# Performance work log

Hardware: AMD Instinct MI355X
Metric: run time of the kernel (lower is better)

The kernel has to match this reference:

```python
import jax, jax.numpy as jnp
import numpy as np

DIM = 1024
LN_EPS = 1e-5

def _layernorm(x, w, b):
    m = jnp.mean(x, axis=-1, keepdims=True)
    v = jnp.mean((x - m) ** 2, axis=-1, keepdims=True)
    return (x - m) * jax.lax.rsqrt(v + LN_EPS) * w + b

def _linear(x, w, b):
    # torch Linear: w is (out, in)
    return jnp.einsum('bsd,od->bso', x, w) + b

def setup_inputs() -> dict:
    key = jax.random.key(0)
    ks = jax.random.split(key, 8)
    d = DIM
    s = 0.02
    return {
        'x': jax.random.normal(ks[0], (4, 4096, d), dtype=jnp.float32),
        'ln1_w': jnp.ones((d,), jnp.float32), 'ln1_b': jnp.zeros((d,), jnp.float32),
        'ln2_w': jnp.ones((d,), jnp.float32), 'ln2_b': jnp.zeros((d,), jnp.float32),
        'gate_w': jax.random.normal(ks[1], (d, d), jnp.float32) * s,
        'gate_b': jnp.zeros((d,), jnp.float32),
        'val_w': jax.random.normal(ks[2], (d, d), jnp.float32) * s,
        'val_b': jnp.zeros((d,), jnp.float32),
        'ffn1_w': jax.random.normal(ks[3], (4 * d, d), jnp.float32) * s,
        'ffn1_b': jnp.zeros((4 * d,), jnp.float32),
        'ffn2_w': jax.random.normal(ks[4], (d, 4 * d), jnp.float32) * s,
        'ffn2_b': jnp.zeros((d,), jnp.float32),
    }

def reference(x, ln1_w, ln1_b, ln2_w, ln2_b, gate_w, gate_b, val_w, val_b, ffn1_w, ffn1_b, ffn2_w, ffn2_b):
    batch, seq_len, dim = x.shape
    h = _layernorm(x, ln1_w, ln1_b)
    g = jax.nn.sigmoid(_linear(h, gate_w, gate_b))
    v = _linear(h, val_w, val_b)
    cumsum_v = jnp.cumsum(g * v, axis=1)
    cumsum_g = jnp.cumsum(g, axis=1) + 1e-6
    position = jnp.arange(1, seq_len + 1, dtype=x.dtype)[None, :, None]  # [1,S,1]
    mem = cumsum_v / (jnp.sqrt(cumsum_g) * jnp.sqrt(position / seq_len + 0.1))
    x = x + mem
    h2 = _layernorm(x, ln2_w, ln2_b)
    ff = _linear(jax.nn.gelu(_linear(h2, ffn1_w, ffn1_b), approximate=False), ffn2_w, ffn2_b)
    return x + ff
```

## Files before the change

### kernel.cpp

```cpp
#include <hip/hip_runtime.h>
#include <cstdint>
#include <cstddef>

#define DIMD 1024
#define SEQ  4096
#define BATCH 4
#define MTOT (BATCH*SEQ)
#define NCHUNK 64
#define CLEN   64

typedef __attribute__((ext_vector_type(8))) short short8;
typedef __attribute__((ext_vector_type(4))) float floatx4;

__device__ __forceinline__ unsigned short f2bf(float f){
  unsigned u = __float_as_uint(f);
  u += 0x7fffu + ((u >> 16) & 1u);
  return (unsigned short)(u >> 16);
}
__device__ __forceinline__ float bf2f(unsigned short u){
  return __uint_as_float((unsigned)u << 16);
}

__device__ __forceinline__ void async16(const void* g, void* l){
  __builtin_amdgcn_global_load_lds(
      (const __attribute__((address_space(1))) void*)g,
      (__attribute__((address_space(3))) void*)l, 16, 0, 0);
}

__global__ void f32_to_bf16_kernel(const float* __restrict__ in,
                                   unsigned short* __restrict__ out, int n){
  int i = (blockIdx.x * 256 + threadIdx.x) * 4;
  if (i < n){
    float4 v = *(const float4*)(in + i);
    uint2 o;
    o.x = (unsigned)f2bf(v.x) | ((unsigned)f2bf(v.y) << 16);
    o.y = (unsigned)f2bf(v.z) | ((unsigned)f2bf(v.w) << 16);
    *(uint2*)(out + i) = o;
  }
}

__global__ __launch_bounds__(256)
void ln_kernel(const float* __restrict__ X, const float* __restrict__ w,
               const float* __restrict__ b, unsigned short* __restrict__ H){
  const int row = blockIdx.x;
  const int tid = threadIdx.x;
  const float4 xv = ((const float4*)(X + (size_t)row * DIMD))[tid];
  float s  = xv.x + xv.y + xv.z + xv.w;
  float ss = xv.x*xv.x + xv.y*xv.y + xv.z*xv.z + xv.w*xv.w;
  #pragma unroll
  for (int o = 32; o; o >>= 1){
    s  += __shfl_down(s, o);
    ss += __shfl_down(ss, o);
  }
  __shared__ float ps[4], pss[4], mv[2];
  const int wid = tid >> 6, lane = tid & 63;
  if (lane == 0){ ps[wid] = s; pss[wid] = ss; }
  __syncthreads();
  if (tid == 0){
    float S1 = ps[0]+ps[1]+ps[2]+ps[3];
    float S2 = pss[0]+pss[1]+pss[2]+pss[3];
    float m = S1 * (1.0f / DIMD);
    float var = S2 * (1.0f / DIMD) - m*m;
    mv[0] = m; mv[1] = rsqrtf(var + 1e-5f);
  }
  __syncthreads();
  const float m = mv[0], rs = mv[1];
  const float4 wv = ((const float4*)w)[tid];
  const float4 bv = ((const float4*)b)[tid];
  float o0 = (xv.x - m) * rs * wv.x + bv.x;
  float o1 = (xv.y - m) * rs * wv.y + bv.y;
  float o2 = (xv.z - m) * rs * wv.z + bv.z;
  float o3 = (xv.w - m) * rs * wv.w + bv.w;
  uint2 o;
  o.x = (unsigned)f2bf(o0) | ((unsigned)f2bf(o1) << 16);
  o.y = (unsigned)f2bf(o2) | ((unsigned)f2bf(o3) << 16);
  ((uint2*)(H + (size_t)row * DIMD))[tid] = o;
}

template<int EPI>
__global__ __launch_bounds__(512, 2)
void gemm256(const unsigned short* __restrict__ A, int lda,
             const unsigned short* __restrict__ Bw, int ldb,
             const float* __restrict__ bias, const float* __restrict__ bias2,
             void* __restrict__ OutP, void* __restrict__ Out2P,
             int ldc, int grid_n, int K)
{
  __shared__ char lds[2][2][32*1024];
  const int tid = threadIdx.x;
  const int bid = ((int)blockIdx.x & 7) * ((int)gridDim.x >> 3) + ((int)blockIdx.x >> 3);
  const int bm = bid / grid_n, bn = bid % grid_n;
  const int row0 = bm * 256, col0 = bn * 256;
  const int wid = tid >> 6, lane = tid & 63;
  const int wr = wid >> 2, wc = wid & 3;
  const int l15 = lane & 15, rq = lane >> 4, l7 = lane & 7;

  const int sbase = ((rq ^ (l7 & 3)) << 4) | (((l7 >> 2) & 1) << 6);

  const int st_r  = tid >> 3;
  const int st_sl = (tid & 7) ^ (st_r & 7);
  const int st_ldsoff = tid * 16;

  const unsigned short* Asrc = A  + (size_t)(row0 + st_r) * lda + st_sl * 8;
  const unsigned short* Bsrc = Bw + (size_t)(col0 + st_r) * ldb + st_sl * 8;

  floatx4 acc[8][4];
  #pragma unroll
  for (int m = 0; m < 8; ++m)
    #pragma unroll
    for (int n = 0; n < 4; ++n)
      acc[m][n] = (floatx4){0.f, 0.f, 0.f, 0.f};

  auto stage = [&](int buf, int k0){
    #pragma unroll
    for (int i = 0; i < 4; ++i)
      async16(Asrc + (size_t)(i * 64) * lda + k0, &lds[buf][0][i * 8192 + st_ldsoff]);
    #pragma unroll
    for (int i = 0; i < 4; ++i)
      async16(Bsrc + (size_t)(i * 64) * ldb + k0, &lds[buf][1][i * 8192 + st_ldsoff]);
  };

  const int nt = K >> 6;
  stage(0, 0);
  asm volatile("s_waitcnt vmcnt(0)" ::: "memory");
  asm volatile("s_barrier" ::: "memory");

  const int arow = wr * 128 + l15;
  const int brow = wc * 64 + l15;

  for (int t = 0; t < nt; ++t){
    const int buf = t & 1;
    const char* La = &lds[buf][0][0];
    const char* Lb = &lds[buf][1][0];
    short8 aF[4][2], bLo[2][2], bHi[2][2];

    #pragma unroll
    for (int mi = 0; mi < 4; ++mi)
      #pragma unroll
      for (int ks = 0; ks < 2; ++ks)
        aF[mi][ks] = *(const short8*)(La + (arow + mi*16) * 128 + (sbase ^ (ks << 6)));
    #pragma unroll
    for (int ni = 0; ni < 2; ++ni)
      #pragma unroll
      for (int ks = 0; ks < 2; ++ks)
        bLo[ni][ks] = *(const short8*)(Lb + (brow + ni*16) * 128 + (sbase ^ (ks << 6)));
    if (t + 1 < nt) stage(buf ^ 1, (t + 1) << 6);
    asm volatile("s_barrier" ::: "memory");
    __builtin_amdgcn_s_setprio(1);
    #pragma unroll
    for (int mi = 0; mi < 4; ++mi)
      #pragma unroll
      for (int ni = 0; ni < 2; ++ni)
        #pragma unroll
        for (int ks = 0; ks < 2; ++ks)
          acc[mi][ni] = __builtin_amdgcn_mfma_f32_16x16x32_bf16(
              aF[mi][ks], bLo[ni][ks], acc[mi][ni], 0, 0, 0);
    __builtin_amdgcn_s_setprio(0);
    asm volatile("s_barrier" ::: "memory");

    #pragma unroll
    for (int ni = 0; ni < 2; ++ni)
      #pragma unroll
      for (int ks = 0; ks < 2; ++ks)
        bHi[ni][ks] = *(const short8*)(Lb + (brow + (2+ni)*16) * 128 + (sbase ^ (ks << 6)));
    asm volatile("s_barrier" ::: "memory");
    __builtin_amdgcn_s_setprio(1);
    #pragma unroll
    for (int mi = 0; mi < 4; ++mi)
      #pragma unroll
      for (int ni = 0; ni < 2; ++ni)
        #pragma unroll
        for (int ks = 0; ks < 2; ++ks)
          acc[mi][2+ni] = __builtin_amdgcn_mfma_f32_16x16x32_bf16(
              aF[mi][ks], bHi[ni][ks], acc[mi][2+ni], 0, 0, 0);
    __builtin_amdgcn_s_setprio(0);
    asm volatile("s_barrier" ::: "memory");

    #pragma unroll
    for (int mi = 0; mi < 4; ++mi)
      #pragma unroll
      for (int ks = 0; ks < 2; ++ks)
        aF[mi][ks] = *(const short8*)(La + (arow + 64 + mi*16) * 128 + (sbase ^ (ks << 6)));
    asm volatile("s_barrier" ::: "memory");
    __builtin_amdgcn_s_setprio(1);
    #pragma unroll
    for (int mi = 0; mi < 4; ++mi)
      #pragma unroll
      for (int ni = 0; ni < 2; ++ni)
        #pragma unroll
        for (int ks = 0; ks < 2; ++ks)
          acc[4+mi][2+ni] = __builtin_amdgcn_mfma_f32_16x16x32_bf16(
              aF[mi][ks], bHi[ni][ks], acc[4+mi][2+ni], 0, 0, 0);
    #pragma unroll
    for (int mi = 0; mi < 4; ++mi)
      #pragma unroll
      for (int ni = 0; ni < 2; ++ni)
        #pragma unroll
        for (int ks = 0; ks < 2; ++ks)
          acc[4+mi][ni] = __builtin_amdgcn_mfma_f32_16x16x32_bf16(
              aF[mi][ks], bLo[ni][ks], acc[4+mi][ni], 0, 0, 0);
    __builtin_amdgcn_s_setprio(0);
    asm volatile("s_waitcnt vmcnt(0)" ::: "memory");
    asm volatile("s_barrier" ::: "memory");
  }

  if constexpr (EPI == 2 || EPI == 5){
    char* slab = &lds[0][0][0] + wid * 8192;
    unsigned short* dst; int colw; int ldout; bool sigm = false;
    const float* bsel;
    if constexpr (EPI == 5){
      const int c0 = col0 + wc * 64;
      if (c0 < 1024){ dst = (unsigned short*)OutP;  colw = c0;        bsel = bias;  sigm = true;  }
      else          { dst = (unsigned short*)Out2P; colw = c0 - 1024; bsel = bias2; sigm = false; }
      ldout = 1024;
    } else {
      dst = (unsigned short*)OutP; colw = col0 + wc * 64; bsel = bias; ldout = ldc;
    }
    const int rdrow = lane >> 3, rdsl = (lane & 7) * 16;
    #pragma unroll
    for (int m = 0; m < 8; ++m){
      #pragma unroll
      for (int n = 0; n < 4; ++n){
        const float bs = bsel[colw + n*16 + l15];
        #pragma unroll
        for (int j = 0; j < 4; ++j){
          const float val = acc[m][n][j] + bs;
          float r;
          if constexpr (EPI == 2){
            r = 0.5f * val * (1.f + erff(val * 0.70710678118f));
          } else {
            r = sigm ? (1.f / (1.f + expf(-val))) : val;
          }
          *(unsigned short*)(slab + (rq*4 + j) * 128 + (n*16 + l15) * 2) = f2bf(r);
        }
      }
      asm volatile("s_waitcnt lgkmcnt(0)" ::: "memory");
      uint4 w0 = *(const uint4*)(slab + rdrow * 128 + rdsl);
      uint4 w1 = *(const uint4*)(slab + (rdrow + 8) * 128 + rdsl);
      asm volatile("s_waitcnt lgkmcnt(0)" ::: "memory");
      const int growb = row0 + wr * 128 + m * 16;
      *(uint4*)((char*)(dst + (size_t)(growb + rdrow) * ldout + colw) + rdsl) = w0;
      *(uint4*)((char*)(dst + (size_t)(growb + rdrow + 8) * ldout + colw) + rdsl) = w1;
    }
  } else {
    #pragma unroll
    for (int n = 0; n < 4; ++n){
      const int col = col0 + wc * 64 + n * 16 + l15;
      const float bs = (EPI == 4) ? 0.f : bias[col];
      #pragma unroll
      for (int m = 0; m < 8; ++m){
        const int rowb = row0 + wr * 128 + m * 16 + rq * 4;
        #pragma unroll
        for (int j = 0; j < 4; ++j){
          const size_t o = (size_t)(rowb + j) * ldc + col;
          float* O = (float*)OutP;
          O[o] = acc[m][n][j] + bs + O[o];
        }
      }
    }
  }
}

__global__ __launch_bounds__(256)
void scan_sums(const unsigned short* __restrict__ G, const unsigned short* __restrict__ V,
               float* __restrict__ SG, float* __restrict__ SGV){
  const int bc = blockIdx.x;
  const int d  = blockIdx.y * 256 + threadIdx.x;
  const int b = bc >> 6, c = bc & 63;
  size_t base = ((size_t)b * SEQ + (size_t)c * CLEN) * DIMD + d;
  float sg = 0.f, sgv = 0.f;
  for (int i = 0; i < CLEN; ++i){
    float g = bf2f(G[base + (size_t)i * DIMD]);
    float v = bf2f(V[base + (size_t)i * DIMD]);
    sg += g; sgv += g * v;
  }
  SG[(size_t)bc * DIMD + d] = sg;
  SGV[(size_t)bc * DIMD + d] = sgv;
}

__global__ __launch_bounds__(256)
void scan_prefix(float* __restrict__ SG, float* __restrict__ SGV){
  const int b = blockIdx.x;
  const int d = blockIdx.y * 256 + threadIdx.x;
  float rg = 0.f, rgv = 0.f;
  for (int c = 0; c < NCHUNK; ++c){
    size_t i = ((size_t)(b * NCHUNK + c)) * DIMD + d;
    float tg = SG[i], tv = SGV[i];
    SG[i] = rg; SGV[i] = rgv;
    rg += tg; rgv += tv;
  }
}

__global__ __launch_bounds__(256)
void scan_final(const unsigned short* __restrict__ G, const unsigned short* __restrict__ V,
                const float* __restrict__ SG, const float* __restrict__ SGV,
                const float* __restrict__ X, float* __restrict__ X2){
  const int bc = blockIdx.x;
  const int d  = blockIdx.y * 256 + threadIdx.x;
  const int b = bc >> 6, c = bc & 63;
  size_t base = ((size_t)b * SEQ + (size_t)c * CLEN) * DIMD + d;
  float rg  = SG[(size_t)bc * DIMD + d];
  float rgv = SGV[(size_t)bc * DIMD + d];
  for (int i = 0; i < CLEN; ++i){
    size_t idx = base + (size_t)i * DIMD;
    float g = bf2f(G[idx]), v = bf2f(V[idx]);
    rg += g; rgv += g * v;
    int s = c * CLEN + i;
    float pf = (float)(s + 1) * (1.0f / SEQ) + 0.1f;
    float mem = rgv * rsqrtf((rg + 1e-6f) * pf);
    X2[idx] = X[idx] + mem;
  }
}

extern "C" void kernel_launch(void* const* d_in, const int* in_sizes, int n_in,
                              void* d_out, int out_size, void* d_ws, size_t ws_size,
                              hipStream_t stream)
{
  const float* x     = (const float*)d_in[0];
  const float* ln1w  = (const float*)d_in[1];
  const float* ln1b  = (const float*)d_in[2];
  const float* ln2w  = (const float*)d_in[3];
  const float* ln2b  = (const float*)d_in[4];
  const float* gatew = (const float*)d_in[5];
  const float* gateb = (const float*)d_in[6];
  const float* valw  = (const float*)d_in[7];
  const float* valb  = (const float*)d_in[8];
  const float* f1w   = (const float*)d_in[9];
  const float* f1b   = (const float*)d_in[10];
  const float* f2w   = (const float*)d_in[11];
  const float* f2b   = (const float*)d_in[12];
  float* out = (float*)d_out;

  const size_t MB = 1024u * 1024u;
  const size_t baseNeed = (size_t)(32+32+32+2+2+8+8)*MB + 2u*BATCH*NCHUNK*DIMD*4 + 4096;
  const bool bigT = (baseNeed + 64u*MB) <= ws_size;

  char* ws = (char*)d_ws;
  size_t off = 0;
  auto alloc = [&](size_t bytes) -> char* {
    char* p = ws + off; off += (bytes + 255) & ~(size_t)255; return p;
  };
  unsigned short* H  = (unsigned short*)alloc((size_t)MTOT * DIMD * 2);
  unsigned short* G  = (unsigned short*)alloc((size_t)MTOT * DIMD * 2);
  unsigned short* V  = (unsigned short*)alloc((size_t)MTOT * DIMD * 2);
  if (bigT) alloc(64u * MB);
  unsigned short* T  = G;
  unsigned short* WGV= (unsigned short*)alloc((size_t)2 * DIMD * DIMD * 2);
  unsigned short* W1 = (unsigned short*)alloc((size_t)4 * DIMD * DIMD * 2);
  unsigned short* W2 = (unsigned short*)alloc((size_t)4 * DIMD * DIMD * 2);
  float* SG  = (float*)alloc((size_t)BATCH * NCHUNK * DIMD * 4);
  float* SGV = (float*)alloc((size_t)BATCH * NCHUNK * DIMD * 4);

  if (off > ws_size) return;

  f32_to_bf16_kernel<<<DIMD*DIMD/1024, 256, 0, stream>>>(gatew, WGV, DIMD*DIMD);
  f32_to_bf16_kernel<<<DIMD*DIMD/1024, 256, 0, stream>>>(valw,  WGV + (size_t)DIMD*DIMD, DIMD*DIMD);
  f32_to_bf16_kernel<<<4*DIMD*DIMD/1024, 256, 0, stream>>>(f1w, W1, 4*DIMD*DIMD);
  f32_to_bf16_kernel<<<4*DIMD*DIMD/1024, 256, 0, stream>>>(f2w, W2, 4*DIMD*DIMD);

  ln_kernel<<<MTOT, 256, 0, stream>>>(x, ln1w, ln1b, H);

  gemm256<5><<<(MTOT/256)*(2048/256), 512, 0, stream>>>(
      H, DIMD, WGV, DIMD, gateb, valb, G, V, 2048, 2048/256, DIMD);

  scan_sums  <<<dim3(BATCH*NCHUNK, DIMD/256), 256, 0, stream>>>(G, V, SG, SGV);
  scan_prefix<<<dim3(BATCH, DIMD/256),        256, 0, stream>>>(SG, SGV);
  scan_final <<<dim3(BATCH*NCHUNK, DIMD/256), 256, 0, stream>>>(G, V, SG, SGV, x, out);

  ln_kernel<<<MTOT, 256, 0, stream>>>(out, ln2w, ln2b, H);

  if (bigT){
    gemm256<2><<<(MTOT/256)*(4096/256), 512, 0, stream>>>(
        H, DIMD, W1, DIMD, f1b, nullptr, T, nullptr, 4*DIMD, 4096/256, DIMD);
    gemm256<3><<<(MTOT/256)*(DIMD/256), 512, 0, stream>>>(
        T, 4*DIMD, W2, 4*DIMD, f2b, nullptr, out, nullptr, DIMD, DIMD/256, 4*DIMD);
  } else {
    for (int c = 0; c < 2; ++c){
      const unsigned short* W1c = W1 + (size_t)c * 2048 * DIMD;
      const unsigned short* W2c = W2 + (size_t)c * 2048;
      gemm256<2><<<(MTOT/256)*(2048/256), 512, 0, stream>>>(
          H, DIMD, W1c, DIMD, f1b + c*2048, nullptr, T, nullptr, 2048, 2048/256, DIMD);
      if (c == 0)
        gemm256<3><<<(MTOT/256)*(DIMD/256), 512, 0, stream>>>(
            T, 2048, W2c, 4*DIMD, f2b, nullptr, out, nullptr, DIMD, DIMD/256, 2048);
      else
        gemm256<4><<<(MTOT/256)*(DIMD/256), 512, 0, stream>>>(
            T, 2048, W2c, 4*DIMD, nullptr, nullptr, out, nullptr, DIMD, DIMD/256, 2048);
    }
  }
}
```

Measured before the change: 564.7 us.

## Use 4-stage LDS pipeline with K=32 tiles in bf16 GEMM

Restructures the GEMM main loop from a double-buffered K=64 tile with several barriers per iteration into a four-buffer ring of K=32 tiles, prefetching three tiles ahead and waiting with vmcnt(8) so global loads overlap more compute. Each iteration now uses one barrier and loads all A and B fragments before issuing the full 8x4 MFMA block. The LDS swizzle changes to fit the 64-byte rows, and the epilogue staging slab gains an XOR swizzle to cut bank conflicts. The risk is more loop iterations and barriers across the full K, and the redundant clamped tail prefetches at the end of the loop.

```diff
diff --git a/kernel.cpp b/kernel.cpp
--- a/kernel.cpp
+++ b/kernel.cpp
@@ -85,23 +85,19 @@
              void* __restrict__ OutP, void* __restrict__ Out2P,
              int ldc, int grid_n, int K)
 {
-  __shared__ char lds[2][2][32*1024];
+  __shared__ char lds[4 * 32768];
   const int tid = threadIdx.x;
   const int bid = ((int)blockIdx.x & 7) * ((int)gridDim.x >> 3) + ((int)blockIdx.x >> 3);
   const int bm = bid / grid_n, bn = bid % grid_n;
   const int row0 = bm * 256, col0 = bn * 256;
   const int wid = tid >> 6, lane = tid & 63;
   const int wr = wid >> 2, wc = wid & 3;
-  const int l15 = lane & 15, rq = lane >> 4, l7 = lane & 7;
-
-  const int sbase = ((rq ^ (l7 & 3)) << 4) | (((l7 >> 2) & 1) << 6);
-
-  const int st_r  = tid >> 3;
-  const int st_sl = (tid & 7) ^ (st_r & 7);
-  const int st_ldsoff = tid * 16;
-
-  const unsigned short* Asrc = A  + (size_t)(row0 + st_r) * lda + st_sl * 8;
-  const unsigned short* Bsrc = Bw + (size_t)(col0 + st_r) * ldb + st_sl * 8;
+  const int l15 = lane & 15, rq = lane >> 4;
+
+  const int st_sl = (tid & 3) ^ ((tid >> 3) & 3);
+  const unsigned short* Asrc = A  + (size_t)(row0 + (tid >> 2)) * lda + st_sl * 8;
+  const unsigned short* Bsrc = Bw + (size_t)(col0 + (tid >> 2)) * ldb + st_sl * 8;
+  const int st_off = tid * 16;
 
   floatx4 acc[8][4];
   #pragma unroll
@@ -110,101 +106,57 @@
     for (int n = 0; n < 4; ++n)
       acc[m][n] = (floatx4){0.f, 0.f, 0.f, 0.f};
 
-  auto stage = [&](int buf, int k0){
-    #pragma unroll
-    for (int i = 0; i < 4; ++i)
-      async16(Asrc + (size_t)(i * 64) * lda + k0, &lds[buf][0][i * 8192 + st_ldsoff]);
-    #pragma unroll
-    for (int i = 0; i < 4; ++i)
-      async16(Bsrc + (size_t)(i * 64) * ldb + k0, &lds[buf][1][i * 8192 + st_ldsoff]);
+  auto stage = [&](int buf, int kt){
+    const int k0 = kt << 5;
+    char* base = lds + buf * 32768;
+    #pragma unroll
+    for (int i = 0; i < 2; ++i)
+      async16(Asrc + (size_t)(i * 128) * lda + k0, base + i * 8192 + st_off);
+    #pragma unroll
+    for (int i = 0; i < 2; ++i)
+      async16(Bsrc + (size_t)(i * 128) * ldb + k0, base + 16384 + i * 8192 + st_off);
   };
 
-  const int nt = K >> 6;
-  stage(0, 0);
-  asm volatile("s_waitcnt vmcnt(0)" ::: "memory");
-  asm volatile("s_barrier" ::: "memory");
-
-  const int arow = wr * 128 + l15;
-  const int brow = wc * 64 + l15;
+  const int nt = K >> 5;
+  stage(0, 0); stage(1, 1); stage(2, 2);
 
   for (int t = 0; t < nt; ++t){
-    const int buf = t & 1;
-    const char* La = &lds[buf][0][0];
-    const char* Lb = &lds[buf][1][0];
-    short8 aF[4][2], bLo[2][2], bHi[2][2];
-
+    asm volatile("s_waitcnt vmcnt(8)" ::: "memory");
+    asm volatile("s_barrier" ::: "memory");
+    const char* La = lds + (t & 3) * 32768;
+    const char* Lb = La + 16384;
+
+    auto LD = [&](const char* Lp, int r)->short8 {
+      return *(const short8*)(Lp + (r << 6) + ((rq ^ ((r >> 1) & 3)) << 4));
+    };
+    short8 a0[4], a1[4], bv[4];
+    #pragma unroll
+    for (int mi = 0; mi < 4; ++mi) a0[mi] = LD(La, wr*128 + mi*16 + l15);
+    #pragma unroll
+    for (int n = 0; n < 4; ++n)    bv[n]  = LD(Lb, wc*64 + n*16 + l15);
+    #pragma unroll
+    for (int mi = 0; mi < 4; ++mi) a1[mi] = LD(La, wr*128 + 64 + mi*16 + l15);
+
+    { const int nxt = (t + 3 < nt) ? t + 3 : nt - 1;
+      stage((t + 3) & 3, nxt); }
+
+    __builtin_amdgcn_s_setprio(1);
     #pragma unroll
     for (int mi = 0; mi < 4; ++mi)
       #pragma unroll
-      for (int ks = 0; ks < 2; ++ks)
-        aF[mi][ks] = *(const short8*)(La + (arow + mi*16) * 128 + (sbase ^ (ks << 6)));
-    #pragma unroll
-    for (int ni = 0; ni < 2; ++ni)
-      #pragma unroll
-      for (int ks = 0; ks < 2; ++ks)
-        bLo[ni][ks] = *(const short8*)(Lb + (brow + ni*16) * 128 + (sbase ^ (ks << 6)));
-    if (t + 1 < nt) stage(buf ^ 1, (t + 1) << 6);
-    asm volatile("s_barrier" ::: "memory");
-    __builtin_amdgcn_s_setprio(1);
+      for (int n = 0; n < 4; ++n)
+        acc[mi][n] = __builtin_amdgcn_mfma_f32_16x16x32_bf16(a0[mi], bv[n], acc[mi][n], 0, 0, 0);
     #pragma unroll
     for (int mi = 0; mi < 4; ++mi)
       #pragma unroll
-      for (int ni = 0; ni < 2; ++ni)
-        #pragma unroll
-        for (int ks = 0; ks < 2; ++ks)
-          acc[mi][ni] = __builtin_amdgcn_mfma_f32_16x16x32_bf16(
-              aF[mi][ks], bLo[ni][ks], acc[mi][ni], 0, 0, 0);
+      for (int n = 0; n < 4; ++n)
+        acc[4+mi][n] = __builtin_amdgcn_mfma_f32_16x16x32_bf16(a1[mi], bv[n], acc[4+mi][n], 0, 0, 0);
     __builtin_amdgcn_s_setprio(0);
+  }
+
+  if constexpr (EPI == 2 || EPI == 5){
     asm volatile("s_barrier" ::: "memory");
-
-    #pragma unroll
-    for (int ni = 0; ni < 2; ++ni)
-      #pragma unroll
-      for (int ks = 0; ks < 2; ++ks)
-        bHi[ni][ks] = *(const short8*)(Lb + (brow + (2+ni)*16) * 128 + (sbase ^ (ks << 6)));
-    asm volatile("s_barrier" ::: "memory");
-    __builtin_amdgcn_s_setprio(1);
-    #pragma unroll
-    for (int mi = 0; mi < 4; ++mi)
-      #pragma unroll
-      for (int ni = 0; ni < 2; ++ni)
-        #pragma unroll
-        for (int ks = 0; ks < 2; ++ks)
-          acc[mi][2+ni] = __builtin_amdgcn_mfma_f32_16x16x32_bf16(
-              aF[mi][ks], bHi[ni][ks], acc[mi][2+ni], 0, 0, 0);
-    __builtin_amdgcn_s_setprio(0);
-    asm volatile("s_barrier" ::: "memory");
-
-    #pragma unroll
-    for (int mi = 0; mi < 4; ++mi)
-      #pragma unroll
-      for (int ks = 0; ks < 2; ++ks)
-        aF[mi][ks] = *(const short8*)(La + (arow + 64 + mi*16) * 128 + (sbase ^ (ks << 6)));
-    asm volatile("s_barrier" ::: "memory");
-    __builtin_amdgcn_s_setprio(1);
-    #pragma unroll
-    for (int mi = 0; mi < 4; ++mi)
-      #pragma unroll
-      for (int ni = 0; ni < 2; ++ni)
-        #pragma unroll
-        for (int ks = 0; ks < 2; ++ks)
-          acc[4+mi][2+ni] = __builtin_amdgcn_mfma_f32_16x16x32_bf16(
-              aF[mi][ks], bHi[ni][ks], acc[4+mi][2+ni], 0, 0, 0);
-    #pragma unroll
-    for (int mi = 0; mi < 4; ++mi)
-      #pragma unroll
-      for (int ni = 0; ni < 2; ++ni)
-        #pragma unroll
-        for (int ks = 0; ks < 2; ++ks)
-          acc[4+mi][ni] = __builtin_amdgcn_mfma_f32_16x16x32_bf16(
-              aF[mi][ks], bLo[ni][ks], acc[4+mi][ni], 0, 0, 0);
-    __builtin_amdgcn_s_setprio(0);
-    asm volatile("s_waitcnt vmcnt(0)" ::: "memory");
-    asm volatile("s_barrier" ::: "memory");
-  }
-
-  if constexpr (EPI == 2 || EPI == 5){
-    char* slab = &lds[0][0][0] + wid * 8192;
+    char* slab = lds + wid * 8192;
     unsigned short* dst; int colw; int ldout; bool sigm = false;
     const float* bsel;
     if constexpr (EPI == 5){
@@ -215,12 +167,16 @@
     } else {
       dst = (unsigned short*)OutP; colw = col0 + wc * 64; bsel = bias; ldout = ldc;
     }
-    const int rdrow = lane >> 3, rdsl = (lane & 7) * 16;
+    const int rdrow = lane >> 3;
+    const int rdoff = rdrow * 128 + (((lane & 7) ^ (rdrow & 7)) << 4);
+    const int rdoff2 = (rdrow + 8) * 128 + (((lane & 7) ^ ((rdrow + 8) & 7)) << 4);
+    const int rdsl = (lane & 7) * 16;
     #pragma unroll
     for (int m = 0; m < 8; ++m){
       #pragma unroll
       for (int n = 0; n < 4; ++n){
         const float bs = bsel[colw + n*16 + l15];
+        const int cchunk = n*2 + (l15 >> 3);
         #pragma unroll
         for (int j = 0; j < 4; ++j){
           const float val = acc[m][n][j] + bs;
@@ -230,12 +186,13 @@
           } else {
             r = sigm ? (1.f / (1.f + expf(-val))) : val;
           }
-          *(unsigned short*)(slab + (rq*4 + j) * 128 + (n*16 + l15) * 2) = f2bf(r);
+          const int rr = rq*4 + j;
+          *(unsigned short*)(slab + rr*128 + ((cchunk ^ (rr & 7)) << 4) + (l15 & 7)*2) = f2bf(r);
         }
       }
       asm volatile("s_waitcnt lgkmcnt(0)" ::: "memory");
-      uint4 w0 = *(const uint4*)(slab + rdrow * 128 + rdsl);
-      uint4 w1 = *(const uint4*)(slab + (rdrow + 8) * 128 + rdsl);
+      uint4 w0 = *(const uint4*)(slab + rdoff);
+      uint4 w1 = *(const uint4*)(slab + rdoff2);
       asm volatile("s_waitcnt lgkmcnt(0)" ::: "memory");
       const int growb = row0 + wr * 128 + m * 16;
       *(uint4*)((char*)(dst + (size_t)(growb + rdrow) * ldout + colw) + rdsl) = w0;
```

Result: faster. 553.3 us (-2.0%).
